# Kernel tuning notes

Measured on AMD Instinct MI355X. Metric: run time of the kernel, lower is better.

## Reference

```python
import jax, jax.numpy as jnp
import numpy as np

N_NODES = 50000
N_EDGES = 800000
LEAKY_SLOPE = 0.01
DROPOUT_P = 0.5


def _graph_conv(src, dst, x, W, b):
    """DGL GraphConv with norm='both': D_out^{-1/2} A D_in^{-1/2} X W + b."""
    n = x.shape[0]
    ones = jnp.ones((src.shape[0],), dtype=x.dtype)
    deg_out = jax.ops.segment_sum(ones, src, num_segments=n)  # out-degree of src nodes
    deg_in = jax.ops.segment_sum(ones, dst, num_segments=n)   # in-degree of dst nodes
    norm_src = jax.lax.rsqrt(jnp.maximum(deg_out, 1.0))
    norm_dst = jax.lax.rsqrt(jnp.maximum(deg_in, 1.0))
    h = (x * norm_src[:, None]) @ W          # apply weight before aggregation
    agg = jax.ops.segment_sum(h[src], dst, num_segments=n)  # SpMM aggregate
    return agg * norm_dst[:, None] + b


def _dropout(x, key, p=DROPOUT_P):
    keep = jax.random.bernoulli(key, 1.0 - p, x.shape)
    return jnp.where(keep, x / (1.0 - p), jnp.zeros((), x.dtype))


def setup_inputs() -> dict:
    key = jax.random.key(0)
    ks = jax.random.split(key, 8)
    features = jax.random.normal(ks[0], (N_NODES, 128), dtype=jnp.float32)
    src = jax.random.randint(ks[1], (N_EDGES,), 0, N_NODES, dtype=jnp.int64)
    dst = jax.random.randint(ks[2], (N_EDGES,), 0, N_NODES, dtype=jnp.int64)
    s1 = 1.0 / np.sqrt(128.0)
    s3 = 1.0 / np.sqrt(128.0)
    W1 = jax.random.normal(ks[3], (128, 128), dtype=jnp.float32) * s1
    W2 = jax.random.normal(ks[4], (128, 128), dtype=jnp.float32) * s1
    W3 = jax.random.normal(ks[5], (128, 64), dtype=jnp.float32) * s3
    b1 = jnp.zeros((128,), dtype=jnp.float32)
    b2 = jnp.zeros((128,), dtype=jnp.float32)
    b3 = jnp.zeros((64,), dtype=jnp.float32)
    return {"features": features, "src": src, "dst": dst,
            "W1": W1, "b1": b1, "W2": W2, "b2": b2, "W3": W3, "b3": b3}


def reference(features, src, dst, W1, b1, W2, b2, W3, b3):
    dk = jax.random.split(jax.random.key(42), 3)
    h = jax.nn.leaky_relu(_graph_conv(src, dst, features, W1, b1), LEAKY_SLOPE)
    h = _dropout(h, dk[0])
    h = jax.nn.leaky_relu(_graph_conv(src, dst, h, W2, b2), LEAKY_SLOPE)
    h = _dropout(h, dk[1])
    h = jax.nn.leaky_relu(_graph_conv(src, dst, h, W3, b3), LEAKY_SLOPE)
    h = _dropout(h, dk[2])
    return h
```

## Files before the change

### kernel.cpp

```cpp
#include <hip/hip_runtime.h>
#include <hip/hip_fp16.h>
#include <stdint.h>

using half8 = __attribute__((ext_vector_type(8))) _Float16;
using f32x4 = __attribute__((ext_vector_type(4))) float;

#define SLOT_CAP 64
#define LDW 136
#define NBINS 50176
#define LWORDS 12544
#define NCHUNK 128

#define TFR(r) { x0 += x1; x1 = (x1 << r) | (x1 >> (32 - r)); x1 ^= x0; }

__host__ __device__ inline void threefry2x32(uint32_t k0, uint32_t k1,
                                             uint32_t c0, uint32_t c1,
                                             uint32_t& o0, uint32_t& o1) {
  uint32_t ks2 = k0 ^ k1 ^ 0x1BD11BDAu;
  uint32_t x0 = c0 + k0, x1 = c1 + k1;
  TFR(13) TFR(15) TFR(26) TFR(6)  x0 += k1;  x1 += ks2 + 1u;
  TFR(17) TFR(29) TFR(16) TFR(24) x0 += ks2; x1 += k0 + 2u;
  TFR(13) TFR(15) TFR(26) TFR(6)  x0 += k0;  x1 += k1 + 3u;
  TFR(17) TFR(29) TFR(16) TFR(24) x0 += k1;  x1 += ks2 + 4u;
  TFR(13) TFR(15) TFR(26) TFR(6)  x0 += ks2; x1 += k0 + 5u;
  o0 = x0; o1 = x1;
}

__device__ inline float tf_uniform(uint32_t k0, uint32_t k1, uint32_t i) {
  uint32_t o0, o1;
  threefry2x32(k0, k1, 0u, i, o0, o1);
  uint32_t bits = o0 ^ o1;
  return __uint_as_float((bits >> 9) | 0x3F800000u) - 1.0f;
}

__device__ inline uint16_t f2h(float f) {
  union { _Float16 h; uint16_t u; } c; c.h = (_Float16)f; return c.u;
}
__device__ inline uint32_t pack2h(float a, float b) {
  return (uint32_t)f2h(a) | ((uint32_t)f2h(b) << 16);
}
__device__ inline __half2 u2h2(uint32_t u) {
  union { uint32_t u; __half2 h; } c; c.u = u; return c.h;
}

__device__ inline void hacc(__half2* a, uint4 r) {
  a[0] = __hadd2(a[0], u2h2(r.x));
  a[1] = __hadd2(a[1], u2h2(r.y));
  a[2] = __hadd2(a[2], u2h2(r.z));
  a[3] = __hadd2(a[3], u2h2(r.w));
}

__global__ __launch_bounds__(256) void build_hist_kernel(
    const int* __restrict__ src, const int* __restrict__ dst,
    uint16_t* __restrict__ histD, uint16_t* __restrict__ histS,
    const float* __restrict__ W1, const float* __restrict__ W2,
    const float* __restrict__ W3, uint16_t* __restrict__ Wt,
    int n, int nE, int HR, int EPB) {
  const int bid = (int)blockIdx.x;
  if (bid >= 512) {
    int i = (bid - 512) * 256 + (int)threadIdx.x;
    float v;
    if (i < 16384) {
      int nr = i >> 7, k = i & 127;
      v = W1[k * 128 + nr];
    } else if (i < 32768) {
      int j = i - 16384, nr = j >> 7, k = j & 127;
      v = W2[k * 128 + nr];
    } else if (i < 40960) {
      int j = i - 32768, nr = j >> 7, k = j & 127;
      v = W3[k * 64 + nr];
    } else return;
    Wt[i] = f2h(v);
    return;
  }

  __shared__ uint32_t bins[LWORDS];
  const bool isSrc = bid >= 256;
  const int c = bid & 127;
  const int h = (bid >> 7) & 1;
  const int lo = h * HR;
  const int* keys = isSrc ? src : dst;
  uint16_t* hist = isSrc ? histS : histD;

  for (int i = threadIdx.x; i < LWORDS; i += 256) bins[i] = 0u;
  __syncthreads();

  const int e0 = c * EPB, e1 = min(e0 + EPB, nE);
  for (int e = e0 + (int)threadIdx.x; e < e1; e += 256) {
    int k = keys[e] - lo;
    if ((unsigned)k < (unsigned)HR)
      atomicAdd(&bins[k >> 1], 1u << ((k & 1) * 16));
  }
  __syncthreads();

  uint32_t* out = (uint32_t*)(hist + (size_t)c * NBINS + lo);
  const int wlim = (min(HR, n - lo) + 1) >> 1;
  for (int i = threadIdx.x; i < wlim; i += 256) out[i] = bins[i];
}

__global__ __launch_bounds__(256) void reduce_kernel(
    uint16_t* __restrict__ histD, const uint16_t* __restrict__ histS,
    int* __restrict__ degin, float* __restrict__ nsrc, int n) {
  const int tid = (int)threadIdx.x;
  const int v = (int)blockIdx.x * 32 + (tid >> 3);
  const int lane8 = tid & 7;
  if (v >= n) return;

  const int c0 = lane8 * 16;
  uint16_t vals[16];
  uint32_t sum = 0;
  #pragma unroll
  for (int j = 0; j < 16; ++j) {
    vals[j] = histD[(size_t)(c0 + j) * NBINS + v];
    sum += vals[j];
  }
  uint32_t run = sum;
  #pragma unroll
  for (int off = 1; off < 8; off <<= 1) {
    uint32_t t = __shfl_up(run, off, 8);
    if (lane8 >= off) run += t;
  }
  const uint32_t total = __shfl(run, 7, 8);
  uint32_t acc = run - sum;
  #pragma unroll
  for (int j = 0; j < 16; ++j) {
    histD[(size_t)(c0 + j) * NBINS + v] = (uint16_t)acc;
    acc += vals[j];
  }
  if (lane8 == 7) degin[v] = (int)total;

  uint32_t s = 0;
  #pragma unroll
  for (int j = 0; j < 16; ++j) s += histS[(size_t)(c0 + j) * NBINS + v];
  #pragma unroll
  for (int off = 1; off < 8; off <<= 1) s += __shfl_xor(s, off, 8);
  if (lane8 == 0) nsrc[v] = rsqrtf(fmaxf((float)s, 1.0f));
}

__global__ __launch_bounds__(256) void scatter_gemm1_kernel(
    const int* __restrict__ src, const int* __restrict__ dst,
    const uint16_t* __restrict__ cumD, uint16_t* __restrict__ edge_slots,
    const float* __restrict__ X, const float* __restrict__ nsrc,
    const uint16_t* __restrict__ Wt1, uint16_t* __restrict__ h1,
    int n, int nE, int HR, int EPB) {
  __shared__ uint32_t bins[LWORDS];
  const int bid = (int)blockIdx.x;

  if (bid < 256) {
    const int c = bid & 127;
    const int h = (bid >> 7) & 1;
    const int lo = h * HR;

    for (int i = threadIdx.x; i < LWORDS; i += 256) bins[i] = 0u;
    __syncthreads();

    const int e0 = c * EPB, e1 = min(e0 + EPB, nE);
    for (int e = e0 + (int)threadIdx.x; e < e1; e += 256) {
      int d = dst[e];
      int k = d - lo;
      if ((unsigned)k < (unsigned)HR) {
        uint32_t old = atomicAdd(&bins[k >> 1], 1u << ((k & 1) * 16));
        int rank = (int)((old >> ((k & 1) * 16)) & 0xFFFFu);
        int pos = (int)cumD[(size_t)c * NBINS + d] + rank;
        if (pos < SLOT_CAP) edge_slots[((size_t)d << 6) + pos] = (uint16_t)src[e];
      }
    }
    return;
  }

  const int r0 = (bid - 256) * 64;
  const int tid = (int)threadIdx.x;
  const int wave = tid >> 6, lane = tid & 63;
  const int wm = wave & 1, wn = wave >> 1;
  const int lane15 = lane & 15, quad = lane >> 4;

  const int rowA0 = r0 + wm * 32 + lane15;
  const int rowA1 = rowA0 + 16;
  const bool v0 = rowA0 < n, v1 = rowA1 < n;

  f32x4 acc[2][4] = {};
  #pragma unroll
  for (int kc = 0; kc < 128; kc += 32) {
    const int ko = kc + quad * 8;
    half8 a0 = {}, a1 = {};
    if (v0) {
      float4 x0 = *(const float4*)&X[(size_t)rowA0 * 128 + ko];
      float4 x1 = *(const float4*)&X[(size_t)rowA0 * 128 + ko + 4];
      a0[0] = (_Float16)x0.x; a0[1] = (_Float16)x0.y;
      a0[2] = (_Float16)x0.z; a0[3] = (_Float16)x0.w;
      a0[4] = (_Float16)x1.x; a0[5] = (_Float16)x1.y;
      a0[6] = (_Float16)x1.z; a0[7] = (_Float16)x1.w;
    }
    if (v1) {
      float4 x0 = *(const float4*)&X[(size_t)rowA1 * 128 + ko];
      float4 x1 = *(const float4*)&X[(size_t)rowA1 * 128 + ko + 4];
      a1[0] = (_Float16)x0.x; a1[1] = (_Float16)x0.y;
      a1[2] = (_Float16)x0.z; a1[3] = (_Float16)x0.w;
      a1[4] = (_Float16)x1.x; a1[5] = (_Float16)x1.y;
      a1[6] = (_Float16)x1.z; a1[7] = (_Float16)x1.w;
    }
    #pragma unroll
    for (int nt = 0; nt < 4; ++nt) {
      int nn = wn * 64 + nt * 16 + lane15;
      half8 b = *(const half8*)&Wt1[nn * 128 + ko];
      acc[0][nt] = __builtin_amdgcn_mfma_f32_16x16x32_f16(a0, b, acc[0][nt], 0, 0, 0);
      acc[1][nt] = __builtin_amdgcn_mfma_f32_16x16x32_f16(a1, b, acc[1][nt], 0, 0, 0);
    }
  }

  #pragma unroll
  for (int mt = 0; mt < 2; ++mt) {
    #pragma unroll
    for (int reg = 0; reg < 4; ++reg) {
      int row = r0 + wm * 32 + mt * 16 + quad * 4 + reg;
      if (row < n) {
        float nsr = nsrc[row];
        #pragma unroll
        for (int nt = 0; nt < 4; ++nt) {
          int col = wn * 64 + nt * 16 + lane15;
          h1[(size_t)row * 128 + col] = f2h(acc[mt][nt][reg] * nsr);
        }
      }
    }
  }
}

template<int NCOLS>
__global__ __launch_bounds__(256) void fuse_gather_gemm_kernel(
    const uint16_t* __restrict__ h_in, const int* __restrict__ degin,
    const uint16_t* __restrict__ edge_slots, const float* __restrict__ nsrc,
    const float* __restrict__ bias, const uint16_t* __restrict__ Wt,
    uint16_t* __restrict__ h_out, uint32_t k0, uint32_t k1, int n) {
  __shared__ uint16_t Xs[32 * LDW];
  __shared__ float ns_s[32];
  const int r0 = (int)blockIdx.x * 32;
  const int tid = (int)threadIdx.x;

  if (tid < 32) {
    int row = r0 + tid;
    ns_s[tid] = (row < n) ? nsrc[row] : 1.0f;
  }

  const int nl = tid >> 3;
  const int node = r0 + nl;
  const int c16 = (tid & 7) * 16;

  if (node < n) {
    __half2 hA[8], hB[8];
    const __half2 z2 = __half2(__float2half(0.f), __float2half(0.f));
    #pragma unroll
    for (int j = 0; j < 8; ++j) { hA[j] = z2; hB[j] = z2; }

    const int dgi = degin[node];
    const int deg = min(dgi, SLOT_CAP);
    const uint16_t* slots = edge_slots + ((size_t)node << 6);
    const uint16_t* hb = h_in + c16;

    int e = 0;
    for (; e + 8 <= deg; e += 8) {
      uint4 sl = *(const uint4*)&slots[e];
      const uint16_t* p0 = hb + ((size_t)(sl.x & 0xFFFF) << 7);
      const uint16_t* p1 = hb + ((size_t)(sl.x >> 16) << 7);
      const uint16_t* p2 = hb + ((size_t)(sl.y & 0xFFFF) << 7);
      const uint16_t* p3 = hb + ((size_t)(sl.y >> 16) << 7);
      const uint16_t* p4 = hb + ((size_t)(sl.z & 0xFFFF) << 7);
      const uint16_t* p5 = hb + ((size_t)(sl.z >> 16) << 7);
      const uint16_t* p6 = hb + ((size_t)(sl.w & 0xFFFF) << 7);
      const uint16_t* p7 = hb + ((size_t)(sl.w >> 16) << 7);
      uint4 a0 = *(const uint4*)p0, b0 = *(const uint4*)(p0 + 8);
      uint4 a1 = *(const uint4*)p1, b1 = *(const uint4*)(p1 + 8);
      uint4 a2 = *(const uint4*)p2, b2 = *(const uint4*)(p2 + 8);
      uint4 a3 = *(const uint4*)p3, b3 = *(const uint4*)(p3 + 8);
      uint4 a4 = *(const uint4*)p4, b4 = *(const uint4*)(p4 + 8);
      uint4 a5 = *(const uint4*)p5, b5 = *(const uint4*)(p5 + 8);
      uint4 a6 = *(const uint4*)p6, b6 = *(const uint4*)(p6 + 8);
      uint4 a7 = *(const uint4*)p7, b7 = *(const uint4*)(p7 + 8);
      hacc(hA, a0); hacc(hA + 4, b0); hacc(hB, a1); hacc(hB + 4, b1);
      hacc(hA, a2); hacc(hA + 4, b2); hacc(hB, a3); hacc(hB + 4, b3);
      hacc(hA, a4); hacc(hA + 4, b4); hacc(hB, a5); hacc(hB + 4, b5);
      hacc(hA, a6); hacc(hA + 4, b6); hacc(hB, a7); hacc(hB + 4, b7);
    }
    for (; e < deg; ++e) {
      const uint16_t* pr = hb + ((size_t)slots[e] << 7);
      uint4 ra = *(const uint4*)pr, rb = *(const uint4*)(pr + 8);
      hacc(hA, ra); hacc(hA + 4, rb);
    }
    #pragma unroll
    for (int j = 0; j < 8; ++j) hA[j] = __hadd2(hA[j], hB[j]);

    float acc[16];
    #pragma unroll
    for (int j = 0; j < 8; ++j) {
      float2 f = __half22float2(hA[j]);
      acc[2 * j] = f.x; acc[2 * j + 1] = f.y;
    }

    const float nd = rsqrtf(fmaxf((float)dgi, 1.0f));
    const float4 b0 = *(const float4*)&bias[c16];
    const float4 b1 = *(const float4*)&bias[c16 + 4];
    const float4 b2 = *(const float4*)&bias[c16 + 8];
    const float4 b3 = *(const float4*)&bias[c16 + 12];
    const float bb[16] = {b0.x, b0.y, b0.z, b0.w, b1.x, b1.y, b1.z, b1.w,
                          b2.x, b2.y, b2.z, b2.w, b3.x, b3.y, b3.z, b3.w};
    const uint32_t i0 = (uint32_t)(node * 128 + c16);

    float o[16];
    #pragma unroll
    for (int j = 0; j < 16; ++j) {
      float v = acc[j] * nd + bb[j];
      v = (v >= 0.f) ? v : 0.01f * v;
      o[j] = (tf_uniform(k0, k1, i0 + (uint32_t)j) < 0.5f) ? v * 2.0f : 0.0f;
    }

    uint4 w0, w1;
    w0.x = pack2h(o[0], o[1]);   w0.y = pack2h(o[2], o[3]);
    w0.z = pack2h(o[4], o[5]);   w0.w = pack2h(o[6], o[7]);
    w1.x = pack2h(o[8], o[9]);   w1.y = pack2h(o[10], o[11]);
    w1.z = pack2h(o[12], o[13]); w1.w = pack2h(o[14], o[15]);
    *(uint4*)&Xs[nl * LDW + c16] = w0;
    *(uint4*)&Xs[nl * LDW + c16 + 8] = w1;
  } else {
    uint4 z = make_uint4(0u, 0u, 0u, 0u);
    *(uint4*)&Xs[nl * LDW + c16] = z;
    *(uint4*)&Xs[nl * LDW + c16 + 8] = z;
  }
  __syncthreads();

  const int wave = tid >> 6, lane = tid & 63;
  const int wm = wave & 1, wn = wave >> 1;
  const int lane15 = lane & 15, quad = lane >> 4;
  constexpr int NT = NCOLS / 32;

  f32x4 acc[NT] = {};
  #pragma unroll
  for (int kc = 0; kc < 128; kc += 32) {
    const int ko = kc + quad * 8;
    half8 a = *(const half8*)&Xs[(wm * 16 + lane15) * LDW + ko];
    #pragma unroll
    for (int nt = 0; nt < NT; ++nt) {
      int nn = wn * (NCOLS / 2) + nt * 16 + lane15;
      half8 b = *(const half8*)&Wt[nn * 128 + ko];
      acc[nt] = __builtin_amdgcn_mfma_f32_16x16x32_f16(a, b, acc[nt], 0, 0, 0);
    }
  }

  #pragma unroll
  for (int nt = 0; nt < NT; ++nt) {
    #pragma unroll
    for (int reg = 0; reg < 4; ++reg) {
      int rl = wm * 16 + quad * 4 + reg;
      int row = r0 + rl;
      if (row < n) {
        int col = wn * (NCOLS / 2) + nt * 16 + lane15;
        h_out[(size_t)row * NCOLS + col] = f2h(acc[nt][reg] * ns_s[rl]);
      }
    }
  }
}

__global__ __launch_bounds__(256) void gather_out_kernel(
    const uint16_t* __restrict__ h3, const int* __restrict__ degin,
    const uint16_t* __restrict__ edge_slots, const float* __restrict__ bias,
    float* __restrict__ out, uint32_t k0, uint32_t k1, int n) {
  const int node = (int)blockIdx.x * 32 + (int)(threadIdx.x >> 3);
  if (node >= n) return;
  const int c8 = (threadIdx.x & 7) * 8;

  const int dgi = degin[node];
  const int deg = min(dgi, SLOT_CAP);
  const uint16_t* slots = edge_slots + ((size_t)node << 6);
  const uint16_t* hb = h3 + c8;

  __half2 hA[4], hB[4];
  const __half2 z2 = __half2(__float2half(0.f), __float2half(0.f));
  #pragma unroll
  for (int j = 0; j < 4; ++j) { hA[j] = z2; hB[j] = z2; }

  int e = 0;
  for (; e + 8 <= deg; e += 8) {
    uint4 sl = *(const uint4*)&slots[e];
    uint4 r0 = *(const uint4*)(hb + ((size_t)(sl.x & 0xFFFF) << 6));
    uint4 r1 = *(const uint4*)(hb + ((size_t)(sl.x >> 16) << 6));
    uint4 r2 = *(const uint4*)(hb + ((size_t)(sl.y & 0xFFFF) << 6));
    uint4 r3 = *(const uint4*)(hb + ((size_t)(sl.y >> 16) << 6));
    uint4 r4 = *(const uint4*)(hb + ((size_t)(sl.z & 0xFFFF) << 6));
    uint4 r5 = *(const uint4*)(hb + ((size_t)(sl.z >> 16) << 6));
    uint4 r6 = *(const uint4*)(hb + ((size_t)(sl.w & 0xFFFF) << 6));
    uint4 r7 = *(const uint4*)(hb + ((size_t)(sl.w >> 16) << 6));
    hacc(hA, r0); hacc(hB, r1); hacc(hA, r2); hacc(hB, r3);
    hacc(hA, r4); hacc(hB, r5); hacc(hA, r6); hacc(hB, r7);
  }
  for (; e < deg; ++e) {
    uint4 r = *(const uint4*)(hb + ((size_t)slots[e] << 6));
    hacc(hA, r);
  }
  #pragma unroll
  for (int j = 0; j < 4; ++j) hA[j] = __hadd2(hA[j], hB[j]);

  float acc[8];
  #pragma unroll
  for (int j = 0; j < 4; ++j) {
    float2 f = __half22float2(hA[j]);
    acc[2 * j] = f.x; acc[2 * j + 1] = f.y;
  }

  const float nd = rsqrtf(fmaxf((float)dgi, 1.0f));
  const float4 b0 = *(const float4*)&bias[c8];
  const float4 b1 = *(const float4*)&bias[c8 + 4];
  const float bb[8] = {b0.x, b0.y, b0.z, b0.w, b1.x, b1.y, b1.z, b1.w};
  const uint32_t i0 = (uint32_t)(node * 64 + c8);

  float o[8];
  #pragma unroll
  for (int j = 0; j < 8; ++j) {
    float v = acc[j] * nd + bb[j];
    v = (v >= 0.f) ? v : 0.01f * v;
    o[j] = (tf_uniform(k0, k1, i0 + (uint32_t)j) < 0.5f) ? v * 2.0f : 0.0f;
  }

  float* op = &out[(size_t)node * 64 + c8];
  *(float4*)op = make_float4(o[0], o[1], o[2], o[3]);
  *(float4*)(op + 4) = make_float4(o[4], o[5], o[6], o[7]);
}

extern "C" void kernel_launch(void* const* d_in, const int* in_sizes, int n_in,
                              void* d_out, int out_size, void* d_ws, size_t ws_size,
                              hipStream_t stream) {
  const float* features = (const float*)d_in[0];
  const int*   src      = (const int*)d_in[1];
  const int*   dst      = (const int*)d_in[2];
  const float* W1       = (const float*)d_in[3];
  const float* b1       = (const float*)d_in[4];
  const float* W2       = (const float*)d_in[5];
  const float* b2       = (const float*)d_in[6];
  const float* W3       = (const float*)d_in[7];
  const float* b3       = (const float*)d_in[8];
  float* out = (float*)d_out;

  const int n  = in_sizes[0] / 128;
  const int nE = in_sizes[1];

  char* p = (char*)d_ws;
  uint16_t* histD      = (uint16_t*)p; p += (size_t)NCHUNK * NBINS * 2;
  uint16_t* histS      = (uint16_t*)p; p += (size_t)NCHUNK * NBINS * 2;
  int* degin           = (int*)p;      p += (size_t)n * 4;
  float* nsrc          = (float*)p;    p += (size_t)n * 4;
  uint16_t* edge_slots = (uint16_t*)p; p += (size_t)n * SLOT_CAP * 2;
  uint16_t* Wt         = (uint16_t*)p; p += 40960 * 2;
  uint16_t* h1         = (uint16_t*)p; p += (size_t)n * 128 * 2;
  uint16_t* h2         = (uint16_t*)p; p += (size_t)n * 128 * 2;
  uint16_t* h3         = (uint16_t*)p;

  uint32_t dk[3][2];
  for (uint32_t i = 0; i < 3; ++i)
    threefry2x32(0u, 42u, 0u, i, dk[i][0], dk[i][1]);

  const int EPB = (nE + NCHUNK - 1) / NCHUNK;
  int HR = ((n + 3) / 2) & ~1;
  if (HR > 2 * LWORDS) HR = 2 * LWORDS;
  const int gb64 = (n + 63) / 64;
  const int gb32 = (n + 31) / 32;

  build_hist_kernel<<<672, 256, 0, stream>>>(src, dst, histD, histS,
                                             W1, W2, W3, Wt, n, nE, HR, EPB);
  reduce_kernel<<<gb32, 256, 0, stream>>>(histD, histS, degin, nsrc, n);
  scatter_gemm1_kernel<<<256 + gb64, 256, 0, stream>>>(
      src, dst, histD, edge_slots, features, nsrc, Wt, h1, n, nE, HR, EPB);
  fuse_gather_gemm_kernel<128><<<gb32, 256, 0, stream>>>(
      h1, degin, edge_slots, nsrc, b1, Wt + 16384, h2, dk[0][0], dk[0][1], n);
  fuse_gather_gemm_kernel<64><<<gb32, 256, 0, stream>>>(
      h2, degin, edge_slots, nsrc, b2, Wt + 32768, h3, dk[1][0], dk[1][1], n);
  gather_out_kernel<<<gb32, 256, 0, stream>>>(
      h3, degin, edge_slots, b3, out, dk[2][0], dk[2][1], n);
}
```

Measured before the change: 267.1 us.

## Split gather into feature-slice kernels and separate GEMM epilogue; finer scatter bins

Replaces the fused gather+GEMM kernels with column-sliced gather kernels that write aggregated features to a panel-major buffer, followed by a separate GEMM kernel that applies normalization, bias, leaky-relu and dropout before the MFMA. Slicing by feature columns is meant to improve L2 locality of the random row gathers, since each block touches only a narrow slice of every neighbor row. The scatter stage now uses 8 dst-range partitions with smaller LDS bins, giving 1024 scatter blocks instead of 256 and raising occupancy. In exchange it adds an extra intermediate buffer round-trip through memory and more kernel launches.

```diff
diff --git a/kernel.cpp b/kernel.cpp
--- a/kernel.cpp
+++ b/kernel.cpp
@@ -6,10 +6,10 @@
 using f32x4 = __attribute__((ext_vector_type(4))) float;
 
 #define SLOT_CAP 64
-#define LDW 136
 #define NBINS 50176
 #define LWORDS 12544
 #define NCHUNK 128
+#define RWORDS 3136
 
 #define TFR(r) { x0 += x1; x1 = (x1 << r) | (x1 >> (32 - r)); x1 ^= x0; }
 
@@ -36,11 +36,11 @@
 __device__ inline uint16_t f2h(float f) {
   union { _Float16 h; uint16_t u; } c; c.h = (_Float16)f; return c.u;
 }
-__device__ inline uint32_t pack2h(float a, float b) {
-  return (uint32_t)f2h(a) | ((uint32_t)f2h(b) << 16);
-}
 __device__ inline __half2 u2h2(uint32_t u) {
   union { uint32_t u; __half2 h; } c; c.u = u; return c.h;
+}
+__device__ inline uint32_t h22u(__half2 h) {
+  union { __half2 h; uint32_t u; } c; c.h = h; return c.u;
 }
 
 __device__ inline void hacc(__half2* a, uint4 r) {
@@ -142,23 +142,23 @@
     const uint16_t* __restrict__ cumD, uint16_t* __restrict__ edge_slots,
     const float* __restrict__ X, const float* __restrict__ nsrc,
     const uint16_t* __restrict__ Wt1, uint16_t* __restrict__ h1,
-    int n, int nE, int HR, int EPB) {
-  __shared__ uint32_t bins[LWORDS];
+    int n, int nE, int RR, int EPB) {
+  __shared__ uint32_t bins[RWORDS];
   const int bid = (int)blockIdx.x;
 
-  if (bid < 256) {
-    const int c = bid & 127;
-    const int h = (bid >> 7) & 1;
-    const int lo = h * HR;
-
-    for (int i = threadIdx.x; i < LWORDS; i += 256) bins[i] = 0u;
+  if (bid < 1024) {
+    const int c = bid >> 3;
+    const int r = bid & 7;
+    const int lo = r * RR;
+
+    for (int i = threadIdx.x; i < RWORDS; i += 256) bins[i] = 0u;
     __syncthreads();
 
     const int e0 = c * EPB, e1 = min(e0 + EPB, nE);
     for (int e = e0 + (int)threadIdx.x; e < e1; e += 256) {
       int d = dst[e];
       int k = d - lo;
-      if ((unsigned)k < (unsigned)HR) {
+      if ((unsigned)k < (unsigned)RR) {
         uint32_t old = atomicAdd(&bins[k >> 1], 1u << ((k & 1) * 16));
         int rank = (int)((old >> ((k & 1) * 16)) & 0xFFFFu);
         int pos = (int)cumD[(size_t)c * NBINS + d] + rank;
@@ -168,7 +168,7 @@
     return;
   }
 
-  const int r0 = (bid - 256) * 64;
+  const int r0 = (bid - 1024) * 64;
   const int tid = (int)threadIdx.x;
   const int wave = tid >> 6, lane = tid & 63;
   const int wm = wave & 1, wn = wave >> 1;
@@ -225,151 +225,63 @@
   }
 }
 
-template<int NCOLS>
-__global__ __launch_bounds__(256) void fuse_gather_gemm_kernel(
+__global__ __launch_bounds__(256) void gather_slice16_kernel(
     const uint16_t* __restrict__ h_in, const int* __restrict__ degin,
-    const uint16_t* __restrict__ edge_slots, const float* __restrict__ nsrc,
-    const float* __restrict__ bias, const uint16_t* __restrict__ Wt,
-    uint16_t* __restrict__ h_out, uint32_t k0, uint32_t k1, int n) {
-  __shared__ uint16_t Xs[32 * LDW];
-  __shared__ float ns_s[32];
-  const int r0 = (int)blockIdx.x * 32;
-  const int tid = (int)threadIdx.x;
-
-  if (tid < 32) {
-    int row = r0 + tid;
-    ns_s[tid] = (row < n) ? nsrc[row] : 1.0f;
-  }
-
-  const int nl = tid >> 3;
-  const int node = r0 + nl;
-  const int c16 = (tid & 7) * 16;
-
-  if (node < n) {
-    __half2 hA[8], hB[8];
-    const __half2 z2 = __half2(__float2half(0.f), __float2half(0.f));
-    #pragma unroll
-    for (int j = 0; j < 8; ++j) { hA[j] = z2; hB[j] = z2; }
-
-    const int dgi = degin[node];
-    const int deg = min(dgi, SLOT_CAP);
-    const uint16_t* slots = edge_slots + ((size_t)node << 6);
-    const uint16_t* hb = h_in + c16;
-
-    int e = 0;
-    for (; e + 8 <= deg; e += 8) {
-      uint4 sl = *(const uint4*)&slots[e];
-      const uint16_t* p0 = hb + ((size_t)(sl.x & 0xFFFF) << 7);
-      const uint16_t* p1 = hb + ((size_t)(sl.x >> 16) << 7);
-      const uint16_t* p2 = hb + ((size_t)(sl.y & 0xFFFF) << 7);
-      const uint16_t* p3 = hb + ((size_t)(sl.y >> 16) << 7);
-      const uint16_t* p4 = hb + ((size_t)(sl.z & 0xFFFF) << 7);
-      const uint16_t* p5 = hb + ((size_t)(sl.z >> 16) << 7);
-      const uint16_t* p6 = hb + ((size_t)(sl.w & 0xFFFF) << 7);
-      const uint16_t* p7 = hb + ((size_t)(sl.w >> 16) << 7);
-      uint4 a0 = *(const uint4*)p0, b0 = *(const uint4*)(p0 + 8);
-      uint4 a1 = *(const uint4*)p1, b1 = *(const uint4*)(p1 + 8);
-      uint4 a2 = *(const uint4*)p2, b2 = *(const uint4*)(p2 + 8);
-      uint4 a3 = *(const uint4*)p3, b3 = *(const uint4*)(p3 + 8);
-      uint4 a4 = *(const uint4*)p4, b4 = *(const uint4*)(p4 + 8);
-      uint4 a5 = *(const uint4*)p5, b5 = *(const uint4*)(p5 + 8);
-      uint4 a6 = *(const uint4*)p6, b6 = *(const uint4*)(p6 + 8);
-      uint4 a7 = *(const uint4*)p7, b7 = *(const uint4*)(p7 + 8);
-      hacc(hA, a0); hacc(hA + 4, b0); hacc(hB, a1); hacc(hB + 4, b1);
-      hacc(hA, a2); hacc(hA + 4, b2); hacc(hB, a3); hacc(hB + 4, b3);
-      hacc(hA, a4); hacc(hA + 4, b4); hacc(hB, a5); hacc(hB + 4, b5);
-      hacc(hA, a6); hacc(hA + 4, b6); hacc(hB, a7); hacc(hB + 4, b7);
-    }
-    for (; e < deg; ++e) {
-      const uint16_t* pr = hb + ((size_t)slots[e] << 7);
-      uint4 ra = *(const uint4*)pr, rb = *(const uint4*)(pr + 8);
-      hacc(hA, ra); hacc(hA + 4, rb);
-    }
-    #pragma unroll
-    for (int j = 0; j < 8; ++j) hA[j] = __hadd2(hA[j], hB[j]);
-
-    float acc[16];
-    #pragma unroll
-    for (int j = 0; j < 8; ++j) {
-      float2 f = __half22float2(hA[j]);
-      acc[2 * j] = f.x; acc[2 * j + 1] = f.y;
-    }
-
-    const float nd = rsqrtf(fmaxf((float)dgi, 1.0f));
-    const float4 b0 = *(const float4*)&bias[c16];
-    const float4 b1 = *(const float4*)&bias[c16 + 4];
-    const float4 b2 = *(const float4*)&bias[c16 + 8];
-    const float4 b3 = *(const float4*)&bias[c16 + 12];
-    const float bb[16] = {b0.x, b0.y, b0.z, b0.w, b1.x, b1.y, b1.z, b1.w,
-                          b2.x, b2.y, b2.z, b2.w, b3.x, b3.y, b3.z, b3.w};
-    const uint32_t i0 = (uint32_t)(node * 128 + c16);
-
-    float o[16];
-    #pragma unroll
-    for (int j = 0; j < 16; ++j) {
-      float v = acc[j] * nd + bb[j];
-      v = (v >= 0.f) ? v : 0.01f * v;
-      o[j] = (tf_uniform(k0, k1, i0 + (uint32_t)j) < 0.5f) ? v * 2.0f : 0.0f;
-    }
-
-    uint4 w0, w1;
-    w0.x = pack2h(o[0], o[1]);   w0.y = pack2h(o[2], o[3]);
-    w0.z = pack2h(o[4], o[5]);   w0.w = pack2h(o[6], o[7]);
-    w1.x = pack2h(o[8], o[9]);   w1.y = pack2h(o[10], o[11]);
-    w1.z = pack2h(o[12], o[13]); w1.w = pack2h(o[14], o[15]);
-    *(uint4*)&Xs[nl * LDW + c16] = w0;
-    *(uint4*)&Xs[nl * LDW + c16 + 8] = w1;
-  } else {
-    uint4 z = make_uint4(0u, 0u, 0u, 0u);
-    *(uint4*)&Xs[nl * LDW + c16] = z;
-    *(uint4*)&Xs[nl * LDW + c16 + 8] = z;
-  }
-  __syncthreads();
-
-  const int wave = tid >> 6, lane = tid & 63;
-  const int wm = wave & 1, wn = wave >> 1;
-  const int lane15 = lane & 15, quad = lane >> 4;
-  constexpr int NT = NCOLS / 32;
-
-  f32x4 acc[NT] = {};
-  #pragma unroll
-  for (int kc = 0; kc < 128; kc += 32) {
-    const int ko = kc + quad * 8;
-    half8 a = *(const half8*)&Xs[(wm * 16 + lane15) * LDW + ko];
-    #pragma unroll
-    for (int nt = 0; nt < NT; ++nt) {
-      int nn = wn * (NCOLS / 2) + nt * 16 + lane15;
-      half8 b = *(const half8*)&Wt[nn * 128 + ko];
-      acc[nt] = __builtin_amdgcn_mfma_f32_16x16x32_f16(a, b, acc[nt], 0, 0, 0);
-    }
-  }
-
-  #pragma unroll
-  for (int nt = 0; nt < NT; ++nt) {
-    #pragma unroll
-    for (int reg = 0; reg < 4; ++reg) {
-      int rl = wm * 16 + quad * 4 + reg;
-      int row = r0 + rl;
-      if (row < n) {
-        int col = wn * (NCOLS / 2) + nt * 16 + lane15;
-        h_out[(size_t)row * NCOLS + col] = f2h(acc[nt][reg] * ns_s[rl]);
-      }
-    }
-  }
-}
-
-__global__ __launch_bounds__(256) void gather_out_kernel(
-    const uint16_t* __restrict__ h3, const int* __restrict__ degin,
-    const uint16_t* __restrict__ edge_slots, const float* __restrict__ bias,
-    float* __restrict__ out, uint32_t k0, uint32_t k1, int n) {
-  const int node = (int)blockIdx.x * 32 + (int)(threadIdx.x >> 3);
+    const uint16_t* __restrict__ edge_slots, uint16_t* __restrict__ agg,
+    int n) {
+  const int slice = (int)blockIdx.x & 7;
+  const int g = (int)blockIdx.x >> 3;
+  const int node = g * 128 + ((int)threadIdx.x >> 1);
+  const int half = (int)threadIdx.x & 1;
   if (node >= n) return;
-  const int c8 = (threadIdx.x & 7) * 8;
-
-  const int dgi = degin[node];
-  const int deg = min(dgi, SLOT_CAP);
+
+  const uint16_t* hb = h_in + slice * 16 + half * 8;
+  const int deg = min(degin[node], SLOT_CAP);
   const uint16_t* slots = edge_slots + ((size_t)node << 6);
-  const uint16_t* hb = h3 + c8;
+
+  __half2 hA[4], hB[4];
+  const __half2 z2 = __half2(__float2half(0.f), __float2half(0.f));
+  #pragma unroll
+  for (int j = 0; j < 4; ++j) { hA[j] = z2; hB[j] = z2; }
+
+  int e = 0;
+  for (; e + 8 <= deg; e += 8) {
+    uint4 sl = *(const uint4*)&slots[e];
+    uint4 r0 = *(const uint4*)(hb + ((size_t)(sl.x & 0xFFFF) << 7));
+    uint4 r1 = *(const uint4*)(hb + ((size_t)(sl.x >> 16) << 7));
+    uint4 r2 = *(const uint4*)(hb + ((size_t)(sl.y & 0xFFFF) << 7));
+    uint4 r3 = *(const uint4*)(hb + ((size_t)(sl.y >> 16) << 7));
+    uint4 r4 = *(const uint4*)(hb + ((size_t)(sl.z & 0xFFFF) << 7));
+    uint4 r5 = *(const uint4*)(hb + ((size_t)(sl.z >> 16) << 7));
+    uint4 r6 = *(const uint4*)(hb + ((size_t)(sl.w & 0xFFFF) << 7));
+    uint4 r7 = *(const uint4*)(hb + ((size_t)(sl.w >> 16) << 7));
+    hacc(hA, r0); hacc(hB, r1); hacc(hA, r2); hacc(hB, r3);
+    hacc(hA, r4); hacc(hB, r5); hacc(hA, r6); hacc(hB, r7);
+  }
+  for (; e < deg; ++e) {
+    uint4 r = *(const uint4*)(hb + ((size_t)slots[e] << 7));
+    hacc(hA, r);
+  }
+  uint4 w;
+  w.x = h22u(__hadd2(hA[0], hB[0]));
+  w.y = h22u(__hadd2(hA[1], hB[1]));
+  w.z = h22u(__hadd2(hA[2], hB[2]));
+  w.w = h22u(__hadd2(hA[3], hB[3]));
+  *(uint4*)&agg[(size_t)slice * n * 16 + (size_t)node * 16 + half * 8] = w;
+}
+
+__global__ __launch_bounds__(256) void gather_slice8_kernel(
+    const uint16_t* __restrict__ h_in, const int* __restrict__ degin,
+    const uint16_t* __restrict__ edge_slots, uint16_t* __restrict__ agg,
+    int n) {
+  const int slice = (int)blockIdx.x & 7;
+  const int g = (int)blockIdx.x >> 3;
+  const int node = g * 256 + (int)threadIdx.x;
+  if (node >= n) return;
+
+  const uint16_t* hb = h_in + slice * 8;
+  const int deg = min(degin[node], SLOT_CAP);
+  const uint16_t* slots = edge_slots + ((size_t)node << 6);
 
   __half2 hA[4], hB[4];
   const __half2 z2 = __half2(__float2half(0.f), __float2half(0.f));
@@ -394,26 +306,99 @@
     uint4 r = *(const uint4*)(hb + ((size_t)slots[e] << 6));
     hacc(hA, r);
   }
-  #pragma unroll
-  for (int j = 0; j < 4; ++j) hA[j] = __hadd2(hA[j], hB[j]);
-
-  float acc[8];
-  #pragma unroll
-  for (int j = 0; j < 4; ++j) {
-    float2 f = __half22float2(hA[j]);
-    acc[2 * j] = f.x; acc[2 * j + 1] = f.y;
-  }
-
-  const float nd = rsqrtf(fmaxf((float)dgi, 1.0f));
-  const float4 b0 = *(const float4*)&bias[c8];
-  const float4 b1 = *(const float4*)&bias[c8 + 4];
+  uint4 w;
+  w.x = h22u(__hadd2(hA[0], hB[0]));
+  w.y = h22u(__hadd2(hA[1], hB[1]));
+  w.z = h22u(__hadd2(hA[2], hB[2]));
+  w.w = h22u(__hadd2(hA[3], hB[3]));
+  *(uint4*)&agg[(size_t)slice * n * 8 + (size_t)node * 8] = w;
+}
+
+template<int NCOLS>
+__global__ __launch_bounds__(256) void gemm_epi_kernel(
+    const uint16_t* __restrict__ agg, const int* __restrict__ degin,
+    const float* __restrict__ nsrc, const float* __restrict__ bias,
+    const uint16_t* __restrict__ Wt, uint16_t* __restrict__ h_out,
+    uint32_t k0, uint32_t k1, int n) {
+  const int r0 = (int)blockIdx.x * 64;
+  const int tid = (int)threadIdx.x;
+  const int wave = tid >> 6, lane = tid & 63;
+  const int lane15 = lane & 15, quad = lane >> 4;
+  const int row = r0 + wave * 16 + lane15;
+  const bool vr = row < n;
+  const float nd = vr ? rsqrtf(fmaxf((float)degin[row], 1.0f)) : 0.f;
+  constexpr int NT = NCOLS / 16;
+
+  f32x4 acc[NT] = {};
+  #pragma unroll
+  for (int kc = 0; kc < 128; kc += 32) {
+    const int ko = kc + quad * 8;
+    half8 a = {};
+    if (vr) {
+      const int panel = ko >> 4, off = ko & 15;
+      uint4 r = *(const uint4*)&agg[(size_t)panel * n * 16 + (size_t)row * 16 + off];
+      float f[8];
+      { float2 t = __half22float2(u2h2(r.x)); f[0] = t.x; f[1] = t.y; }
+      { float2 t = __half22float2(u2h2(r.y)); f[2] = t.x; f[3] = t.y; }
+      { float2 t = __half22float2(u2h2(r.z)); f[4] = t.x; f[5] = t.y; }
+      { float2 t = __half22float2(u2h2(r.w)); f[6] = t.x; f[7] = t.y; }
+      float4 bA = *(const float4*)&bias[ko];
+      float4 bB = *(const float4*)&bias[ko + 4];
+      const float bb[8] = {bA.x, bA.y, bA.z, bA.w, bB.x, bB.y, bB.z, bB.w};
+      const uint32_t i0 = (uint32_t)(row * 128 + ko);
+      #pragma unroll
+      for (int j = 0; j < 8; ++j) {
+        float v = f[j] * nd + bb[j];
+        v = (v >= 0.f) ? v : 0.01f * v;
+        v = (tf_uniform(k0, k1, i0 + (uint32_t)j) < 0.5f) ? v * 2.0f : 0.0f;
+        a[j] = (_Float16)v;
+      }
+    }
+    #pragma unroll
+    for (int nt = 0; nt < NT; ++nt) {
+      half8 b = *(const half8*)&Wt[(nt * 16 + lane15) * 128 + ko];
+      acc[nt] = __builtin_amdgcn_mfma_f32_16x16x32_f16(a, b, acc[nt], 0, 0, 0);
+    }
+  }
+
+  #pragma unroll
+  for (int reg = 0; reg < 4; ++reg) {
+    int orow = r0 + wave * 16 + quad * 4 + reg;
+    if (orow < n) {
+      float nsr = nsrc[orow];
+      #pragma unroll
+      for (int nt = 0; nt < NT; ++nt)
+        h_out[(size_t)orow * NCOLS + nt * 16 + lane15] = f2h(acc[nt][reg] * nsr);
+    }
+  }
+}
+
+__global__ __launch_bounds__(256) void epi_out_kernel(
+    const uint16_t* __restrict__ agg, const int* __restrict__ degin,
+    const float* __restrict__ bias, float* __restrict__ out,
+    uint32_t k0, uint32_t k1, int n) {
+  const int node = (int)blockIdx.x * 32 + ((int)threadIdx.x >> 3);
+  if (node >= n) return;
+  const int p = (int)threadIdx.x & 7;
+
+  uint4 r = *(const uint4*)&agg[(size_t)p * n * 8 + (size_t)node * 8];
+  float f[8];
+  { float2 t = __half22float2(u2h2(r.x)); f[0] = t.x; f[1] = t.y; }
+  { float2 t = __half22float2(u2h2(r.y)); f[2] = t.x; f[3] = t.y; }
+  { float2 t = __half22float2(u2h2(r.z)); f[4] = t.x; f[5] = t.y; }
+  { float2 t = __half22float2(u2h2(r.w)); f[6] = t.x; f[7] = t.y; }
+
+  const float nd = rsqrtf(fmaxf((float)degin[node], 1.0f));
+  const int c8 = p * 8;
+  float4 b0 = *(const float4*)&bias[c8];
+  float4 b1 = *(const float4*)&bias[c8 + 4];
   const float bb[8] = {b0.x, b0.y, b0.z, b0.w, b1.x, b1.y, b1.z, b1.w};
   const uint32_t i0 = (uint32_t)(node * 64 + c8);
 
   float o[8];
   #pragma unroll
   for (int j = 0; j < 8; ++j) {
-    float v = acc[j] * nd + bb[j];
+    float v = f[j] * nd + bb[j];
     v = (v >= 0.f) ? v : 0.01f * v;
     o[j] = (tf_uniform(k0, k1, i0 + (uint32_t)j) < 0.5f) ? v * 2.0f : 0.0f;
   }
@@ -449,7 +434,8 @@
   uint16_t* Wt         = (uint16_t*)p; p += 40960 * 2;
   uint16_t* h1         = (uint16_t*)p; p += (size_t)n * 128 * 2;
   uint16_t* h2         = (uint16_t*)p; p += (size_t)n * 128 * 2;
-  uint16_t* h3         = (uint16_t*)p;
+  uint16_t* h3         = (uint16_t*)p; p += (size_t)n * 64 * 2;
+  uint16_t* agg        = (uint16_t*)p;
 
   uint32_t dk[3][2];
   for (uint32_t i = 0; i < 3; ++i)
@@ -458,18 +444,24 @@
   const int EPB = (nE + NCHUNK - 1) / NCHUNK;
   int HR = ((n + 3) / 2) & ~1;
   if (HR > 2 * LWORDS) HR = 2 * LWORDS;
+  int RR = ((n + 15) / 8) & ~1;
+  if (RR > 2 * RWORDS) RR = 2 * RWORDS;
   const int gb64 = (n + 63) / 64;
-  const int gb32 = (n + 31) / 32;
+  const int gs16 = 8 * ((n + 127) / 128);
+  const int gs8  = 8 * ((n + 255) / 256);
 
   build_hist_kernel<<<672, 256, 0, stream>>>(src, dst, histD, histS,
                                              W1, W2, W3, Wt, n, nE, HR, EPB);
-  reduce_kernel<<<gb32, 256, 0, stream>>>(histD, histS, degin, nsrc, n);
-  scatter_gemm1_kernel<<<256 + gb64, 256, 0, stream>>>(
-      src, dst, histD, edge_slots, features, nsrc, Wt, h1, n, nE, HR, EPB);
-  fuse_gather_gemm_kernel<128><<<gb32, 256, 0, stream>>>(
-      h1, degin, edge_slots, nsrc, b1, Wt + 16384, h2, dk[0][0], dk[0][1], n);
-  fuse_gather_gemm_kernel<64><<<gb32, 256, 0, stream>>>(
-      h2, degin, edge_slots, nsrc, b2, Wt + 32768, h3, dk[1][0], dk[1][1], n);
-  gather_out_kernel<<<gb32, 256, 0, stream>>>(
-      h3, degin, edge_slots, b3, out, dk[2][0], dk[2][1], n);
-}
+  reduce_kernel<<<(n + 31) / 32, 256, 0, stream>>>(histD, histS, degin, nsrc, n);
+  scatter_gemm1_kernel<<<1024 + gb64, 256, 0, stream>>>(
+      src, dst, histD, edge_slots, features, nsrc, Wt, h1, n, nE, RR, EPB);
+  gather_slice16_kernel<<<gs16, 256, 0, stream>>>(h1, degin, edge_slots, agg, n);
+  gemm_epi_kernel<128><<<gb64, 256, 0, stream>>>(
+      agg, degin, nsrc, b1, Wt + 16384, h2, dk[0][0], dk[0][1], n);
+  gather_slice16_kernel<<<gs16, 256, 0, stream>>>(h2, degin, edge_slots, agg, n);
+  gemm_epi_kernel<64><<<gb64, 256, 0, stream>>>(
+      agg, degin, nsrc, b2, Wt + 32768, h3, dk[1][0], dk[1][1], n);
+  gather_slice8_kernel<<<gs8, 256, 0, stream>>>(h3, degin, edge_slots, agg, n);
+  epi_out_kernel<<<(n + 31) / 32, 256, 0, stream>>>(
+      agg, degin, b3, out, dk[2][0], dk[2][1], n);
+}
```

After: 476.6 us. 1.78x slower.
